# Optimization experiments

Hardware: AMD Instinct MI355X
Metric: run time of the kernel (lower is better)

The kernel has to match this reference:

```python
import jax, jax.numpy as jnp
import numpy as np

N_EMBD = 1024
HEAD_SIZE = 128
B, T = 8, 2048


def apply_rope(x):
    # x: (B, T, D); rotate interleaved pairs, matching torch view(B,T,D//2,2)
    b, t, d = x.shape
    freqs = 1.0 / (10000.0 ** (jnp.arange(0, d, 2, dtype=jnp.float32) / d))  # (D//2,)
    angles = jnp.arange(t, dtype=jnp.float32)[:, None] * freqs[None, :]      # (T, D//2)
    cos_a = jnp.cos(angles).astype(x.dtype)
    sin_a = jnp.sin(angles).astype(x.dtype)
    xr = x.reshape(b, t, d // 2, 2)
    x0, x1 = xr[..., 0], xr[..., 1]
    rot = jnp.stack([x0 * cos_a - x1 * sin_a, x0 * sin_a + x1 * cos_a], axis=-1)
    return rot.reshape(b, t, d)


def setup_inputs() -> dict:
    key = jax.random.key(0)
    kx, kq, kk, kv = jax.random.split(key, 4)
    x = jax.random.normal(kx, (B, T, N_EMBD), dtype=jnp.float32)
    scale = 0.02
    Wq = jax.random.normal(kq, (N_EMBD, HEAD_SIZE), dtype=jnp.float32) * scale
    Wk = jax.random.normal(kk, (N_EMBD, HEAD_SIZE), dtype=jnp.float32) * scale
    Wv = jax.random.normal(kv, (N_EMBD, HEAD_SIZE), dtype=jnp.float32) * scale
    return {"x": x, "Wq": Wq, "Wk": Wk, "Wv": Wv}


def reference(x, Wq, Wk, Wv):
    # QKV projections (bias=False)
    q = x @ Wq  # (B, T, H)
    k = x @ Wk
    v = x @ Wv
    q = apply_rope(q)
    k = apply_rope(k)
    d = k.shape[-1]
    wei = jnp.einsum('bqd,bkd->bqk', q, k) * (d ** -0.5)  # (B, T, T)
    causal = jnp.tril(jnp.ones((q.shape[1], q.shape[1]), dtype=bool))
    wei = jnp.where(causal, wei, jnp.finfo(wei.dtype).min)
    wei = jax.nn.softmax(wei, axis=-1)
    out = jnp.einsum('bqk,bkd->bqd', wei, v)  # (B, T, H)
    return out
```

## Files before the change

### kernel.cpp

```cpp
#include <hip/hip_runtime.h>
#include <math.h>

#define BB 8
#define TT 2048
#define EE 1024
#define DD 128

typedef _Float16 f16x8 __attribute__((ext_vector_type(8)));
typedef _Float16 f16x4 __attribute__((ext_vector_type(4)));
typedef float    f32x4 __attribute__((ext_vector_type(4)));
typedef float    f32x16 __attribute__((ext_vector_type(16)));

#define QSCALE 0.12752406f

__device__ __forceinline__ void gl_lds16(const _Float16* g, _Float16* l)
{
    __builtin_amdgcn_global_load_lds(
        (const __attribute__((address_space(1))) void*)g,
        (__attribute__((address_space(3))) void*)l, 16, 0, 0);
}


__global__ __launch_bounds__(256)
void wt_prep_kernel(const float* __restrict__ Wq,
                    const float* __restrict__ Wk,
                    const float* __restrict__ Wv,
                    _Float16* __restrict__ Wb)
{
    int gid = blockIdx.x * 256 + threadIdx.x;
    int kc  = gid / 768;
    int rem = gid - kc * 768;
    int ns  = rem >> 6;
    int ln  = rem & 63;
    int n   = ns * 32 + (ln & 31);
    int k0  = kc * 16 + (ln >> 5) * 8;
    const float* __restrict__ W = (n < 128) ? Wq : (n < 256) ? Wk : Wv;
    int nl = n & 127;
    f16x8 w;
#pragma unroll
    for (int j = 0; j < 8; j++)
        w[j] = (_Float16)W[(size_t)(k0 + j) * DD + nl];
    *(f16x8*)&Wb[(size_t)gid * 8] = w;
}

__global__ __launch_bounds__(512)
void proj_rope_kernel(const float* __restrict__ x,
                      const _Float16* __restrict__ Wb,
                      _Float16* __restrict__ Qb,
                      _Float16* __restrict__ Ka,
                      _Float16* __restrict__ Va)
{
    const int r0   = blockIdx.x * 64;
    const int tid  = threadIdx.x;
    const int wave = tid >> 6;
    const int lane = tid & 63;
    const int half = lane >> 5;
    const int col  = lane & 31;
    const int wave_m = wave & 1;
    const int wave_n = wave >> 1;

    __shared__ _Float16 Xb[2][4096];
    __shared__ _Float16 WtL[2][24576];
    __shared__ _Float16 Out[64][136];

    f32x16 acc[3];
#pragma unroll
    for (int s = 0; s < 3; s++) acc[s] = (f32x16)0.f;

    const int sr = tid >> 3;
    const int sc = (tid & 7) * 4;
    const float* __restrict__ xp = &x[(size_t)(r0 + sr) * EE + sc];
    const int sm = sr >> 5, rr = sr & 31;
    const int w0 = (((sc      >> 4) * 2 + sm) << 9) + ((rr + 32 * ((sc       >> 3) & 1)) << 3) + (sc & 7);
    const int w1 = ((((sc+32) >> 4) * 2 + sm) << 9) + ((rr + 32 * (((sc+32)  >> 3) & 1)) << 3) + (sc & 7);

    const _Float16* __restrict__ wsrc = Wb + (size_t)(wave * 6) * 512 + lane * 8;

    {
        float4 pa0 = *(const float4*)(xp);
        float4 pa1 = *(const float4*)(xp + 32);
        f16x4 h0 = { (_Float16)pa0.x, (_Float16)pa0.y, (_Float16)pa0.z, (_Float16)pa0.w };
        f16x4 h1 = { (_Float16)pa1.x, (_Float16)pa1.y, (_Float16)pa1.z, (_Float16)pa1.w };
        *(f16x4*)&Xb[0][w0] = h0;
        *(f16x4*)&Xb[0][w1] = h1;
    }
#pragma unroll
    for (int i = 0; i < 6; i++)
        gl_lds16(wsrc + (size_t)i * 512, &WtL[0][(wave * 6 + i) * 512]);
    float4 na0 = *(const float4*)(xp + 64);
    float4 na1 = *(const float4*)(xp + 96);

    for (int it = 0; it < 16; it++) {
        const int buf = it & 1;
        __syncthreads();
        float4 nx0, nx1;
        if (it + 2 < 16) {
            nx0 = *(const float4*)(xp + (it + 2) * 64);
            nx1 = *(const float4*)(xp + (it + 2) * 64 + 32);
        }
        if (it + 1 < 16) {
            const _Float16* ws = wsrc + (size_t)(it + 1) * 24576;
            _Float16* wd = &WtL[buf ^ 1][(wave * 6) * 512];
#pragma unroll
            for (int i = 0; i < 6; i++)
                gl_lds16(ws + (size_t)i * 512, wd + i * 512);
        }
#pragma unroll
        for (int kc = 0; kc < 4; kc++) {
            f16x8 a = *(f16x8*)&Xb[buf][((kc * 2 + wave_m) << 9) + lane * 8];
#pragma unroll
            for (int s = 0; s < 3; s++) {
                f16x8 b = *(f16x8*)&WtL[buf][(kc * 12 + wave_n * 3 + s) * 512 + lane * 8];
                acc[s] = __builtin_amdgcn_mfma_f32_32x32x16_f16(a, b, acc[s], 0, 0, 0);
            }
        }
        if (it + 1 < 16) {
            f16x4 h0 = { (_Float16)na0.x, (_Float16)na0.y, (_Float16)na0.z, (_Float16)na0.w };
            f16x4 h1 = { (_Float16)na1.x, (_Float16)na1.y, (_Float16)na1.z, (_Float16)na1.w };
            *(f16x4*)&Xb[buf ^ 1][w0] = h0;
            *(f16x4*)&Xb[buf ^ 1][w1] = h1;
            na0 = nx0; na1 = nx1;
        }
    }

    const int bidx = r0 >> 11;
    const int t0   = r0 & (TT - 1);

    for (int p = 0; p < 3; p++) {
        __syncthreads();
#pragma unroll
        for (int s = 0; s < 3; s++) {
            int gs = wave_n * 3 + s;
            if ((gs >> 2) != p) continue;
            int dcol = (gs & 3) * 32 + col;
            float f = 0.f;
            if (p < 2)
                f = __powf(10000.0f, -(float)(dcol & ~1) * (1.0f / 128.0f));
#pragma unroll
            for (int rg = 0; rg < 16; rg++) {
                int mrow = wave_m * 32 + (rg & 3) + 8 * (rg >> 2) + 4 * half;
                float av = acc[s][rg];
                float res;
                if (p < 2) {
                    float ap = __shfl_xor(av, 1);
                    float sa, ca;
                    __sincosf((float)(t0 + mrow) * f, &sa, &ca);
                    res = av * ca + ap * ((dcol & 1) ? sa : -sa);
                    if (p == 0) res *= QSCALE;
                } else {
                    res = av;
                }
                Out[mrow][dcol] = (_Float16)res;
            }
        }
        __syncthreads();
        if (p < 2) {
            _Float16* __restrict__ dst = (p == 0) ? Qb : Ka;
#pragma unroll
            for (int jj = 0; jj < 2; jj++) {
                int cid = tid + 512 * jj;
                int sl = cid >> 9, kc = (cid >> 6) & 7, ln = cid & 63;
                f16x8 v8 = *(f16x8*)&Out[sl * 32 + (ln & 31)][kc * 16 + (ln >> 5) * 8];
                size_t ga = ((((size_t)bidx * 64 + (t0 >> 5) + sl) * 8 + kc) * 64 + ln) * 8;
                *(f16x8*)&dst[ga] = v8;
            }
        } else {
#pragma unroll
            for (int jj = 0; jj < 2; jj++) {
                int cid = tid + 512 * jj;
                int kcl = cid >> 8, ds = (cid >> 6) & 3, ln = cid & 63;
                f16x8 vv;
#pragma unroll
                for (int e = 0; e < 8; e++)
                    vv[e] = Out[kcl * 16 + (ln >> 5) * 8 + e][ds * 32 + (ln & 31)];
                size_t ga = ((((size_t)bidx * 128 + (t0 >> 4) + kcl) * 4 + ds) * 64 + ln) * 8;
                *(f16x8*)&Va[ga] = vv;
            }
        }
    }
}

__global__ __launch_bounds__(256)
void attn_kernel(const _Float16* __restrict__ Qb,
                 const _Float16* __restrict__ Ka,
                 const _Float16* __restrict__ Va,
                 _Float16* __restrict__ opart,
                 float* __restrict__ mpart,
                 float* __restrict__ lpart)
{
    const int b  = blockIdx.y;
    const int v_ = 39 - blockIdx.x;
    int xt, c;
    if (v_ < 4)       { xt = v_;                  c = 0; }
    else if (v_ < 12) { xt = 4 + ((v_ - 4) >> 1); c = (v_ - 4) & 1; }
    else if (v_ < 24) { xt = 8 + (v_ - 12) / 3;   c = (v_ - 12) % 3; }
    else              { xt = 12 + ((v_ - 24) >> 2); c = (v_ - 24) & 3; }
    const int q0 = xt * 128;
    const int nt = 2 * xt + 2;
    const int kt_begin = c * 8;
    const int kt_end   = (kt_begin + 8 < nt) ? (kt_begin + 8) : nt;

    const int tid  = threadIdx.x;
    const int wave = tid >> 6;
    const int lane = tid & 63;
    const int half = lane >> 5;
    const int col  = lane & 31;

    __shared__ _Float16 Kb[8192];
    __shared__ _Float16 Vb[8192];
    __shared__ _Float16 Ps[4][32][72];

    const _Float16* __restrict__ kst = Ka + (size_t)b * 64 * 4096;
    const _Float16* __restrict__ vst = Va + (size_t)b * 128 * 2048;

    const int qg = q0 + wave * 32 + col;
    f16x8 qb[8];
#pragma unroll
    for (int kc = 0; kc < 8; kc++)
        qb[kc] = *(const f16x8*)&Qb[((((size_t)b * 64 + xt * 4 + wave) * 8 + kc) * 64 + lane) * 8];

    f32x16 Of[4];
#pragma unroll
    for (int t = 0; t < 4; t++) Of[t] = (f32x16)0.f;
    float m_ = -1e30f, l_ = 0.f;

    f16x8 kr[4], vr[4];
    {
        const _Float16* kp = kst + (size_t)kt_begin * 8192;
        const _Float16* vp = vst + (size_t)kt_begin * 8192;
#pragma unroll
        for (int i = 0; i < 4; i++) kr[i] = *(const f16x8*)&kp[(tid + 256 * i) * 8];
#pragma unroll
        for (int i = 0; i < 4; i++) vr[i] = *(const f16x8*)&vp[(tid + 256 * i) * 8];
    }

    for (int kt = kt_begin; kt < kt_end; kt++) {
        const int kb0 = kt * 64;
        __syncthreads();
#pragma unroll
        for (int i = 0; i < 4; i++) *(f16x8*)&Kb[(tid + 256 * i) * 8] = kr[i];
#pragma unroll
        for (int i = 0; i < 4; i++) *(f16x8*)&Vb[(tid + 256 * i) * 8] = vr[i];
        __syncthreads();
        if (kt + 1 < kt_end) {
            const _Float16* kp = kst + (size_t)(kt + 1) * 8192;
            const _Float16* vp = vst + (size_t)(kt + 1) * 8192;
#pragma unroll
            for (int i = 0; i < 4; i++) kr[i] = *(const f16x8*)&kp[(tid + 256 * i) * 8];
#pragma unroll
            for (int i = 0; i < 4; i++) vr[i] = *(const f16x8*)&vp[(tid + 256 * i) * 8];
        }

        f32x16 sf[2];
#pragma unroll
        for (int g = 0; g < 2; g++) {
            sf[g] = (f32x16)0.f;
#pragma unroll
            for (int kc = 0; kc < 8; kc++) {
                f16x8 kf = *(f16x8*)&Kb[((g * 8 + kc) * 64 + lane) * 8];
                sf[g] = __builtin_amdgcn_mfma_f32_32x32x16_f16(kf, qb[kc], sf[g], 0, 0, 0);
            }
        }

        const bool diag = (kt >= 2 * xt);
        float mloc = -1e30f;
#pragma unroll
        for (int g = 0; g < 2; g++)
#pragma unroll
            for (int rg = 0; rg < 16; rg++) {
                int key = kb0 + g * 32 + (rg & 3) + 8 * (rg >> 2) + 4 * half;
                float val = sf[g][rg];
                val = (!diag || key <= qg) ? val : -1e30f;
                sf[g][rg] = val;
                mloc = fmaxf(mloc, val);
            }
        mloc = fmaxf(mloc, __shfl_xor(mloc, 32));
        float mnew  = fmaxf(m_, mloc);
        float alpha = __builtin_amdgcn_exp2f(m_ - mnew);
        float ps = 0.f;
#pragma unroll
        for (int g = 0; g < 2; g++) {
#pragma unroll
            for (int rc = 0; rc < 4; rc++) {
                f16x4 p4;
#pragma unroll
                for (int rr = 0; rr < 4; rr++) {
                    float p = __builtin_amdgcn_exp2f(sf[g][4 * rc + rr] - mnew);
                    ps += p;
                    p4[rr] = (_Float16)p;
                }
                *(f16x4*)&Ps[wave][col][g * 32 + 8 * rc + 4 * half] = p4;
            }
        }
        ps += __shfl_xor(ps, 32);
        l_ = l_ * alpha + ps;
        m_ = mnew;
#pragma unroll
        for (int t = 0; t < 4; t++) Of[t] *= alpha;

        f16x8 pb[4];
#pragma unroll
        for (int kc = 0; kc < 4; kc++)
            pb[kc] = *(f16x8*)&Ps[wave][col][kc * 16 + half * 8];
#pragma unroll
        for (int t = 0; t < 4; t++) {
#pragma unroll
            for (int kcl = 0; kcl < 4; kcl++) {
                f16x8 vf = *(f16x8*)&Vb[((kcl * 4 + t) * 64 + lane) * 8];
                Of[t] = __builtin_amdgcn_mfma_f32_32x32x16_f16(vf, pb[kcl], Of[t], 0, 0, 0);
            }
        }
    }

    const int slot = (b * 16 + xt) * 4 + c;
    _Float16* op = opart + ((size_t)slot * 128 + wave * 32 + col) * DD;
#pragma unroll
    for (int t = 0; t < 4; t++) {
#pragma unroll
        for (int rc = 0; rc < 4; rc++) {
            f16x4 o4 = { (_Float16)Of[t][4 * rc + 0], (_Float16)Of[t][4 * rc + 1],
                         (_Float16)Of[t][4 * rc + 2], (_Float16)Of[t][4 * rc + 3] };
            *(f16x4*)&op[t * 32 + 8 * rc + 4 * half] = o4;
        }
    }
    if (half == 0) {
        mpart[slot * 128 + wave * 32 + col] = m_;
        lpart[slot * 128 + wave * 32 + col] = l_;
    }
}

__global__ __launch_bounds__(256)
void combine_kernel(const _Float16* __restrict__ opart,
                    const float* __restrict__ mpart,
                    const float* __restrict__ lpart,
                    float* __restrict__ out)
{
    int gid = blockIdx.x * 256 + threadIdx.x;
    int dg  = (gid & 15) * 8;
    int t   = gid >> 4;
    int b   = t >> 11;
    int tl  = t & (TT - 1);
    int xt  = tl >> 7;
    int rl  = tl & 127;
    int np  = (2 * xt + 2 + 7) >> 3;
    int sb  = (b * 16 + xt) * 4;

    float mm = -1e30f;
    for (int j = 0; j < np; j++)
        mm = fmaxf(mm, mpart[(sb + j) * 128 + rl]);

    float den = 0.f;
    float a0 = 0.f, a1 = 0.f, a2 = 0.f, a3 = 0.f;
    float a4 = 0.f, a5 = 0.f, a6 = 0.f, a7 = 0.f;
    for (int j = 0; j < np; j++) {
        float w = __builtin_amdgcn_exp2f(mpart[(sb + j) * 128 + rl] - mm);
        den += w * lpart[(sb + j) * 128 + rl];
        f16x8 o = *(const f16x8*)&opart[((size_t)(sb + j) * 128 + rl) * DD + dg];
        a0 += w * (float)o[0]; a1 += w * (float)o[1];
        a2 += w * (float)o[2]; a3 += w * (float)o[3];
        a4 += w * (float)o[4]; a5 += w * (float)o[5];
        a6 += w * (float)o[6]; a7 += w * (float)o[7];
    }
    float inv = 1.f / den;
    float4 r0 = { a0 * inv, a1 * inv, a2 * inv, a3 * inv };
    float4 r1 = { a4 * inv, a5 * inv, a6 * inv, a7 * inv };
    float* op = &out[(size_t)t * DD + dg];
    *(float4*)(op)     = r0;
    *(float4*)(op + 4) = r1;
}

extern "C" void kernel_launch(void* const* d_in, const int* in_sizes, int n_in,
                              void* d_out, int out_size, void* d_ws, size_t ws_size,
                              hipStream_t stream)
{
    const float* x  = (const float*)d_in[0];
    const float* Wq = (const float*)d_in[1];
    const float* Wk = (const float*)d_in[2];
    const float* Wv = (const float*)d_in[3];
    float* out = (float*)d_out;

    const size_t NTOK = (size_t)BB * TT;
    _Float16* Qb = (_Float16*)d_ws;
    _Float16* Ka = Qb + NTOK * DD;
    _Float16* Va = Ka + NTOK * DD;
    _Float16* Wb = Va + NTOK * DD;
    _Float16* opart = Wb + (size_t)384 * EE;
    float* mp = (float*)(opart + (size_t)512 * 128 * DD);
    float* lp = mp + 512 * 128;

    wt_prep_kernel<<<dim3(192), dim3(256), 0, stream>>>(Wq, Wk, Wv, Wb);
    proj_rope_kernel<<<dim3(256), dim3(512), 0, stream>>>(x, Wb, Qb, Ka, Va);
    attn_kernel<<<dim3(40, BB), dim3(256), 0, stream>>>(Qb, Ka, Va, opart, mp, lp);
    combine_kernel<<<dim3((int)(NTOK * DD / 8 / 256)), dim3(256), 0, stream>>>(opart, mp, lp, out);
}
```

Baseline: 155.4 us.

## Split each attention block's key tile across two wave groups with separate partial softmax

The attention kernel now runs 512 threads: eight waves, where each query wave-group of four handles one 32-key half of every 64-key tile. Each half keeps its own running max, sum and output partial and writes them to separate slots. The combine kernel merges twice as many partials. This doubles the waves per block to hide MFMA and memory latency, at the cost of twice the partial output traffic and a larger combine step.

```diff
diff --git a/kernel.cpp b/kernel.cpp
--- a/kernel.cpp
+++ b/kernel.cpp
@@ -180,7 +180,7 @@
     }
 }
 
-__global__ __launch_bounds__(256)
+__global__ __launch_bounds__(512)
 void attn_kernel(const _Float16* __restrict__ Qb,
                  const _Float16* __restrict__ Ka,
                  const _Float16* __restrict__ Va,
@@ -205,92 +205,85 @@
     const int lane = tid & 63;
     const int half = lane >> 5;
     const int col  = lane & 31;
+    const int wq   = wave & 3;
+    const int wk   = wave >> 2;
 
     __shared__ _Float16 Kb[8192];
     __shared__ _Float16 Vb[8192];
-    __shared__ _Float16 Ps[4][32][72];
+    __shared__ _Float16 Ps[8][32][36];
 
     const _Float16* __restrict__ kst = Ka + (size_t)b * 64 * 4096;
     const _Float16* __restrict__ vst = Va + (size_t)b * 128 * 2048;
 
-    const int qg = q0 + wave * 32 + col;
+    const int qg = q0 + wq * 32 + col;
     f16x8 qb[8];
 #pragma unroll
     for (int kc = 0; kc < 8; kc++)
-        qb[kc] = *(const f16x8*)&Qb[((((size_t)b * 64 + xt * 4 + wave) * 8 + kc) * 64 + lane) * 8];
+        qb[kc] = *(const f16x8*)&Qb[((((size_t)b * 64 + xt * 4 + wq) * 8 + kc) * 64 + lane) * 8];
 
     f32x16 Of[4];
 #pragma unroll
     for (int t = 0; t < 4; t++) Of[t] = (f32x16)0.f;
     float m_ = -1e30f, l_ = 0.f;
 
-    f16x8 kr[4], vr[4];
+    f16x8 kr[2], vr[2];
     {
         const _Float16* kp = kst + (size_t)kt_begin * 8192;
         const _Float16* vp = vst + (size_t)kt_begin * 8192;
 #pragma unroll
-        for (int i = 0; i < 4; i++) kr[i] = *(const f16x8*)&kp[(tid + 256 * i) * 8];
-#pragma unroll
-        for (int i = 0; i < 4; i++) vr[i] = *(const f16x8*)&vp[(tid + 256 * i) * 8];
+        for (int i = 0; i < 2; i++) kr[i] = *(const f16x8*)&kp[(tid + 512 * i) * 8];
+#pragma unroll
+        for (int i = 0; i < 2; i++) vr[i] = *(const f16x8*)&vp[(tid + 512 * i) * 8];
     }
 
     for (int kt = kt_begin; kt < kt_end; kt++) {
         const int kb0 = kt * 64;
         __syncthreads();
 #pragma unroll
-        for (int i = 0; i < 4; i++) *(f16x8*)&Kb[(tid + 256 * i) * 8] = kr[i];
-#pragma unroll
-        for (int i = 0; i < 4; i++) *(f16x8*)&Vb[(tid + 256 * i) * 8] = vr[i];
+        for (int i = 0; i < 2; i++) *(f16x8*)&Kb[(tid + 512 * i) * 8] = kr[i];
+#pragma unroll
+        for (int i = 0; i < 2; i++) *(f16x8*)&Vb[(tid + 512 * i) * 8] = vr[i];
         __syncthreads();
         if (kt + 1 < kt_end) {
             const _Float16* kp = kst + (size_t)(kt + 1) * 8192;
             const _Float16* vp = vst + (size_t)(kt + 1) * 8192;
 #pragma unroll
-            for (int i = 0; i < 4; i++) kr[i] = *(const f16x8*)&kp[(tid + 256 * i) * 8];
-#pragma unroll
-            for (int i = 0; i < 4; i++) vr[i] = *(const f16x8*)&vp[(tid + 256 * i) * 8];
-        }
-
-        f32x16 sf[2];
-#pragma unroll
-        for (int g = 0; g < 2; g++) {
-            sf[g] = (f32x16)0.f;
-#pragma unroll
-            for (int kc = 0; kc < 8; kc++) {
-                f16x8 kf = *(f16x8*)&Kb[((g * 8 + kc) * 64 + lane) * 8];
-                sf[g] = __builtin_amdgcn_mfma_f32_32x32x16_f16(kf, qb[kc], sf[g], 0, 0, 0);
-            }
+            for (int i = 0; i < 2; i++) kr[i] = *(const f16x8*)&kp[(tid + 512 * i) * 8];
+#pragma unroll
+            for (int i = 0; i < 2; i++) vr[i] = *(const f16x8*)&vp[(tid + 512 * i) * 8];
+        }
+
+        f32x16 sf = (f32x16)0.f;
+#pragma unroll
+        for (int kc = 0; kc < 8; kc++) {
+            f16x8 kf = *(f16x8*)&Kb[((wk * 8 + kc) * 64 + lane) * 8];
+            sf = __builtin_amdgcn_mfma_f32_32x32x16_f16(kf, qb[kc], sf, 0, 0, 0);
         }
 
         const bool diag = (kt >= 2 * xt);
         float mloc = -1e30f;
 #pragma unroll
-        for (int g = 0; g < 2; g++)
-#pragma unroll
-            for (int rg = 0; rg < 16; rg++) {
-                int key = kb0 + g * 32 + (rg & 3) + 8 * (rg >> 2) + 4 * half;
-                float val = sf[g][rg];
-                val = (!diag || key <= qg) ? val : -1e30f;
-                sf[g][rg] = val;
-                mloc = fmaxf(mloc, val);
-            }
+        for (int rg = 0; rg < 16; rg++) {
+            int key = kb0 + wk * 32 + (rg & 3) + 8 * (rg >> 2) + 4 * half;
+            float val = sf[rg];
+            val = (!diag || key <= qg) ? val : -1e30f;
+            sf[rg] = val;
+            mloc = fmaxf(mloc, val);
+        }
         mloc = fmaxf(mloc, __shfl_xor(mloc, 32));
         float mnew  = fmaxf(m_, mloc);
         float alpha = __builtin_amdgcn_exp2f(m_ - mnew);
         float ps = 0.f;
 #pragma unroll
-        for (int g = 0; g < 2; g++) {
-#pragma unroll
-            for (int rc = 0; rc < 4; rc++) {
-                f16x4 p4;
-#pragma unroll
-                for (int rr = 0; rr < 4; rr++) {
-                    float p = __builtin_amdgcn_exp2f(sf[g][4 * rc + rr] - mnew);
-                    ps += p;
-                    p4[rr] = (_Float16)p;
-                }
-                *(f16x4*)&Ps[wave][col][g * 32 + 8 * rc + 4 * half] = p4;
-            }
+        for (int rc = 0; rc < 4; rc++) {
+            f16x4 p4;
+#pragma unroll
+            for (int rr = 0; rr < 4; rr++) {
+                float p = __builtin_amdgcn_exp2f(sf[4 * rc + rr] - mnew);
+                ps += p;
+                p4[rr] = (_Float16)p;
+            }
+            *(f16x4*)&Ps[wave][col][8 * rc + 4 * half] = p4;
         }
         ps += __shfl_xor(ps, 32);
         l_ = l_ * alpha + ps;
@@ -298,22 +291,22 @@
 #pragma unroll
         for (int t = 0; t < 4; t++) Of[t] *= alpha;
 
-        f16x8 pb[4];
-#pragma unroll
-        for (int kc = 0; kc < 4; kc++)
+        f16x8 pb[2];
+#pragma unroll
+        for (int kc = 0; kc < 2; kc++)
             pb[kc] = *(f16x8*)&Ps[wave][col][kc * 16 + half * 8];
 #pragma unroll
         for (int t = 0; t < 4; t++) {
 #pragma unroll
-            for (int kcl = 0; kcl < 4; kcl++) {
-                f16x8 vf = *(f16x8*)&Vb[((kcl * 4 + t) * 64 + lane) * 8];
-                Of[t] = __builtin_amdgcn_mfma_f32_32x32x16_f16(vf, pb[kcl], Of[t], 0, 0, 0);
-            }
-        }
-    }
-
-    const int slot = (b * 16 + xt) * 4 + c;
-    _Float16* op = opart + ((size_t)slot * 128 + wave * 32 + col) * DD;
+            for (int kc = 0; kc < 2; kc++) {
+                f16x8 vf = *(f16x8*)&Vb[(((wk * 2 + kc) * 4 + t) * 64 + lane) * 8];
+                Of[t] = __builtin_amdgcn_mfma_f32_32x32x16_f16(vf, pb[kc], Of[t], 0, 0, 0);
+            }
+        }
+    }
+
+    const int slot = (((b * 16 + xt) * 4) + c) * 2 + wk;
+    _Float16* op = opart + ((size_t)slot * 128 + wq * 32 + col) * DD;
 #pragma unroll
     for (int t = 0; t < 4; t++) {
 #pragma unroll
@@ -324,8 +317,8 @@
         }
     }
     if (half == 0) {
-        mpart[slot * 128 + wave * 32 + col] = m_;
-        lpart[slot * 128 + wave * 32 + col] = l_;
+        mpart[slot * 128 + wq * 32 + col] = m_;
+        lpart[slot * 128 + wq * 32 + col] = l_;
     }
 }
 
@@ -342,8 +335,8 @@
     int tl  = t & (TT - 1);
     int xt  = tl >> 7;
     int rl  = tl & 127;
-    int np  = (2 * xt + 2 + 7) >> 3;
-    int sb  = (b * 16 + xt) * 4;
+    int np  = ((2 * xt + 2 + 7) >> 3) * 2;
+    int sb  = (b * 16 + xt) * 8;
 
     float mm = -1e30f;
     for (int j = 0; j < np; j++)
@@ -385,11 +378,11 @@
     _Float16* Va = Ka + NTOK * DD;
     _Float16* Wb = Va + NTOK * DD;
     _Float16* opart = Wb + (size_t)384 * EE;
-    float* mp = (float*)(opart + (size_t)512 * 128 * DD);
-    float* lp = mp + 512 * 128;
+    float* mp = (float*)(opart + (size_t)1024 * 128 * DD);
+    float* lp = mp + 1024 * 128;
 
     wt_prep_kernel<<<dim3(192), dim3(256), 0, stream>>>(Wq, Wk, Wv, Wb);
     proj_rope_kernel<<<dim3(256), dim3(512), 0, stream>>>(x, Wb, Qb, Ka, Va);
-    attn_kernel<<<dim3(40, BB), dim3(256), 0, stream>>>(Qb, Ka, Va, opart, mp, lp);
+    attn_kernel<<<dim3(40, BB), dim3(512), 0, stream>>>(Qb, Ka, Va, opart, mp, lp);
     combine_kernel<<<dim3((int)(NTOK * DD / 8 / 256)), dim3(256), 0, stream>>>(opart, mp, lp, out);
 }
```

Result: slower. 163.9 us (+5.5%).
